# Kernel optimization log

Measured on AMD Instinct MI355X. Metric: run time of the kernel, lower is better.

Reference implementation:

```python
import jax, jax.numpy as jnp
import numpy as np

B, TE, TD, H = 4, 1024, 512, 128


def setup_inputs() -> dict:
    key = jax.random.key(0)
    k1, k2, k3, k4, k5 = jax.random.split(key, 5)
    return {
        "encoder_out": jax.random.normal(k1, (B, TE, H), dtype=jnp.float32),
        "decoder_out": jax.random.normal(k2, (B, TD, H), dtype=jnp.float32),
        "W_a": jax.random.normal(k3, (H, H), dtype=jnp.float32) * 0.05,
        "U_a": jax.random.normal(k4, (H, H), dtype=jnp.float32) * 0.05,
        "V_a": jax.random.normal(k5, (H, 1), dtype=jnp.float32) * 0.05,
    }


def reference(encoder_out, decoder_out, W_a, U_a, V_a):
    # Bahdanau additive attention, vectorized over all decoder steps at once.
    # (The original K.rnn loop has no true recurrence; steps are independent.)
    W_s = jnp.einsum('bth,hk->btk', encoder_out, W_a)   # [B, Te, H]
    U_h = jnp.einsum('bdh,hk->bdk', decoder_out, U_a)   # [B, Td, H]
    # energies: v^T tanh(W s_t + U h_d) -> [B, Td, Te]
    tanh_arg = jnp.tanh(W_s[:, None, :, :] + U_h[:, :, None, :])  # [B, Td, Te, H]
    e = jnp.einsum('bdth,ho->bdt', tanh_arg, V_a)
    e = jax.nn.softmax(e, axis=-1)                      # attention weights [B, Td, Te]
    # context vectors: weighted sum over encoder positions -> [B, Td, H]
    c = jnp.einsum('bdt,bth->bdh', e, encoder_out)
    return (c, e)
```

## Files before the change

kernel.cpp:

```cpp
#include <hip/hip_runtime.h>

#define BB    4
#define TE    1024
#define TD    512
#define HH    128
#define DTILE 4
#define TTILE 64
#define ESTR  (TE + 8)
#define LOG2E 1.4426950408889634f

typedef float f32x2 __attribute__((ext_vector_type(2)));

__device__ __forceinline__ f32x2 pk_fma(f32x2 a, f32x2 b, f32x2 c) {
    return __builtin_elementwise_fma(a, b, c);
}

__device__ __forceinline__ float tanh_eval(float x) {
    float e = __builtin_amdgcn_exp2f(2.0f * LOG2E * x);
    return 1.0f - 2.0f * __builtin_amdgcn_rcpf(e + 1.0f);
}

__global__ __launch_bounds__(256) void proj_gemm(
    const float* __restrict__ enc, const float* __restrict__ dec,
    const float* __restrict__ Wa,  const float* __restrict__ Ua,
    float* __restrict__ out)
{
    __shared__ float Xs[64 * 33];
    __shared__ float Ws[32 * 64];

    const int tid = threadIdx.x;
    const int rt = blockIdx.x >> 1, ch = blockIdx.x & 1;
    const int r0 = rt * 64, c0 = ch * 64;

    const float* X; const float* W; int rX0;
    if (r0 < BB * TE) { X = enc; W = Wa; rX0 = r0; }
    else              { X = dec; W = Ua; rX0 = r0 - BB * TE; }

    const int c4 = tid & 15;
    const int rg = tid >> 4;

    float4 a0 = {0,0,0,0}, a1 = a0, a2 = a0, a3 = a0;

    for (int kc = 0; kc < 4; ++kc) {
        #pragma unroll
        for (int i = 0; i < 2; ++i) {
            int idx = tid + i * 256;
            int r  = idx >> 3, k4 = idx & 7;
            *(float4*)&Xs[r * 33 + k4 * 4] =
                *(const float4*)&X[(rX0 + r) * HH + kc * 32 + k4 * 4];
            int kk = idx >> 4, cc = idx & 15;
            *(float4*)&Ws[kk * 64 + cc * 4] =
                *(const float4*)&W[(kc * 32 + kk) * HH + c0 + cc * 4];
        }
        __syncthreads();
        #pragma unroll 8
        for (int k = 0; k < 32; ++k) {
            float4 wv = *(const float4*)&Ws[k * 64 + c4 * 4];
            float x0 = Xs[(rg * 4 + 0) * 33 + k];
            float x1 = Xs[(rg * 4 + 1) * 33 + k];
            float x2 = Xs[(rg * 4 + 2) * 33 + k];
            float x3 = Xs[(rg * 4 + 3) * 33 + k];
            a0.x = fmaf(x0, wv.x, a0.x); a0.y = fmaf(x0, wv.y, a0.y);
            a0.z = fmaf(x0, wv.z, a0.z); a0.w = fmaf(x0, wv.w, a0.w);
            a1.x = fmaf(x1, wv.x, a1.x); a1.y = fmaf(x1, wv.y, a1.y);
            a1.z = fmaf(x1, wv.z, a1.z); a1.w = fmaf(x1, wv.w, a1.w);
            a2.x = fmaf(x2, wv.x, a2.x); a2.y = fmaf(x2, wv.y, a2.y);
            a2.z = fmaf(x2, wv.z, a2.z); a2.w = fmaf(x2, wv.w, a2.w);
            a3.x = fmaf(x3, wv.x, a3.x); a3.y = fmaf(x3, wv.y, a3.y);
            a3.z = fmaf(x3, wv.z, a3.z); a3.w = fmaf(x3, wv.w, a3.w);
        }
        __syncthreads();
    }

    float4 accs[4] = {a0, a1, a2, a3};
    #pragma unroll
    for (int j = 0; j < 4; ++j) {
        float4 o = accs[j];
        o.x = tanh_eval(o.x); o.y = tanh_eval(o.y);
        o.z = tanh_eval(o.z); o.w = tanh_eval(o.w);
        *(float4*)&out[(r0 + rg * 4 + j) * HH + c0 + c4 * 4] = o;
    }
}

__global__ __launch_bounds__(512, 4) void attn_fused(
    const float* __restrict__ enc,
    const float* __restrict__ ta,
    const float* __restrict__ tb,
    const float* __restrict__ Va,
    float* __restrict__ c_out,
    float* __restrict__ e_out)
{
    __shared__ float e_s[DTILE * ESTR];
    __shared__ float c_red[8 * DTILE * HH];

    const int tid = threadIdx.x;
    const int l   = tid & 63;
    const int w   = tid >> 6;
    const int b   = blockIdx.x >> 7;
    const int d0  = (blockIdx.x & 127) * DTILE;

    {
        const int g  = l >> 3;
        const int hl = l & 7;
        const int dl = g & 3;
        const int rh = g >> 2;

        f32x2 Bl[4], Bh[4], Pl[4], Ph[4], Vl[4], Vh[4];
        #pragma unroll
        for (int j = 0; j < 4; ++j) {
            float4 vv = *(const float4*)&Va[(j * 8 + hl) * 4];
            float4 bb = *(const float4*)&tb[((size_t)b * TD + d0 + dl) * HH + (j * 8 + hl) * 4];
            Vl[j] = (f32x2){vv.x, vv.y};  Vh[j] = (f32x2){vv.z, vv.w};
            Bl[j] = (f32x2){bb.x, bb.y};  Bh[j] = (f32x2){bb.z, bb.w};
            Pl[j] = Vl[j] * Bl[j];        Ph[j] = Vh[j] * Bh[j];
        }

        const float* ta_b = ta + (size_t)b * TE * HH;

        auto rowOf = [&](int i) {
            return ((i >> 2) << 6) + w * 8 + ((i & 3) << 1) + rh;
        };

        float4 A0[4], A1[4];
        auto loadA = [&](int i, float4 (&A)[4]) {
            const float* base = ta_b + (size_t)rowOf(i) * HH;
            #pragma unroll
            for (int j = 0; j < 4; ++j)
                A[j] = *(const float4*)&base[(j * 8 + hl) * 4];
        };

        auto p1c = [&](int i, float4 (&A)[4]) {
            const f32x2 one2 = {1.0f, 1.0f};
            f32x2 n2[8], d2[8];
            #pragma unroll
            for (int j = 0; j < 4; ++j) {
                f32x2 Al = (f32x2){A[j].x, A[j].y};
                f32x2 Ah = (f32x2){A[j].z, A[j].w};
                n2[2 * j]     = pk_fma(Vl[j], Al, Pl[j]);
                n2[2 * j + 1] = pk_fma(Vh[j], Ah, Ph[j]);
                d2[2 * j]     = pk_fma(Al, Bl[j], one2);
                d2[2 * j + 1] = pk_fma(Ah, Bh[j], one2);
            }
            #pragma unroll
            for (int s = 4; s >= 1; s >>= 1) {
                #pragma unroll
                for (int k = 0; k < s; ++k) {
                    n2[k] = pk_fma(n2[2 * k], d2[2 * k + 1], n2[2 * k + 1] * d2[2 * k]);
                    d2[k] = d2[2 * k] * d2[2 * k + 1];
                }
            }
            float num = n2[0].x * d2[0].y + n2[0].y * d2[0].x;
            float den = d2[0].x * d2[0].y;
            float e = num * __builtin_amdgcn_rcpf(den);
            e += __shfl_xor(e, 1);
            e += __shfl_xor(e, 2);
            e += __shfl_xor(e, 4);
            if (hl == 0) e_s[dl * ESTR + rowOf(i)] = e;
        };

        loadA(0, A0);
        #pragma unroll 1
        for (int i = 0; i < 62; i += 2) {
            loadA(i + 1, A1);
            p1c(i, A0);
            loadA(i + 2, A0);
            p1c(i + 1, A1);
        }
        loadA(63, A1);
        p1c(62, A0);
        p1c(63, A1);
    }
    __syncthreads();

    {
        const int d2 = w & 3, hf = w >> 2;
        float ev[16];
        float m = -3.0e38f;
        #pragma unroll
        for (int i = 0; i < 16; ++i) {
            ev[i] = e_s[d2 * ESTR + i * 64 + l];
            m = fmaxf(m, ev[i]);
        }
        #pragma unroll
        for (int off = 32; off; off >>= 1) m = fmaxf(m, __shfl_xor(m, off));
        float s = 0.f;
        #pragma unroll
        for (int i = 0; i < 16; ++i) {
            ev[i] = __builtin_amdgcn_exp2f((ev[i] - m) * LOG2E);
            s += ev[i];
        }
        #pragma unroll
        for (int off = 32; off; off >>= 1) s += __shfl_xor(s, off);
        float inv = __builtin_amdgcn_rcpf(s);

        __syncthreads();
        float* eo = e_out + ((size_t)b * TD + d0 + d2) * TE;
        #pragma unroll
        for (int i = 0; i < 8; ++i) {
            int ii = hf * 8 + i;
            float p = ev[ii] * inv;
            e_s[d2 * ESTR + ii * 64 + l] = p;
            eo[ii * 64 + l] = p;
        }
        __syncthreads();
    }

    const int h4 = l & 31, tsub = l >> 5;
    f32x2 accL[DTILE], accH[DTILE];
    #pragma unroll
    for (int d = 0; d < DTILE; ++d) {
        accL[d] = (f32x2){0.f, 0.f};
        accH[d] = (f32x2){0.f, 0.f};
    }

    {
        const float* enc_w = enc + ((size_t)b * TE + w * 8) * HH;
        float4 X0[4], X1[4];

        auto loadX = [&](int tt, float4 (&X)[4]) {
            const float* base = enc_w + (size_t)tt * TTILE * HH;
            #pragma unroll
            for (int k = 0; k < 4; ++k)
                X[k] = *(const float4*)&base[(tsub * 4 + k) * HH + h4 * 4];
        };

        auto p3c = [&](int tt, float4 (&X)[4]) {
            float4 ep[DTILE];
            #pragma unroll
            for (int d = 0; d < DTILE; ++d)
                ep[d] = *(const float4*)&e_s[d * ESTR + tt * TTILE + w * 8 + tsub * 4];
            #pragma unroll
            for (int k = 0; k < 4; ++k) {
                f32x2 xL = (f32x2){X[k].x, X[k].y};
                f32x2 xH = (f32x2){X[k].z, X[k].w};
                #pragma unroll
                for (int d = 0; d < DTILE; ++d) {
                    float p = k == 0 ? ep[d].x : k == 1 ? ep[d].y
                            : k == 2 ? ep[d].z : ep[d].w;
                    f32x2 pv = (f32x2){p, p};
                    accL[d] = pk_fma(pv, xL, accL[d]);
                    accH[d] = pk_fma(pv, xH, accH[d]);
                }
            }
        };

        loadX(0, X0);
        #pragma unroll 1
        for (int tt = 0; tt < 14; tt += 2) {
            loadX(tt + 1, X1);
            p3c(tt, X0);
            loadX(tt + 2, X0);
            p3c(tt + 1, X1);
        }
        loadX(15, X1);
        p3c(14, X0);
        p3c(15, X1);
    }

    float4 acc4[DTILE];
    #pragma unroll
    for (int d = 0; d < DTILE; ++d)
        acc4[d] = make_float4(accL[d].x, accL[d].y, accH[d].x, accH[d].y);
    #pragma unroll
    for (int d = 0; d < DTILE; ++d) {
        acc4[d].x += __shfl_xor(acc4[d].x, 32);
        acc4[d].y += __shfl_xor(acc4[d].y, 32);
        acc4[d].z += __shfl_xor(acc4[d].z, 32);
        acc4[d].w += __shfl_xor(acc4[d].w, 32);
    }
    if (tsub == 0) {
        #pragma unroll
        for (int d = 0; d < DTILE; ++d)
            *(float4*)&c_red[(w * DTILE + d) * HH + h4 * 4] = acc4[d];
    }
    __syncthreads();

    if (w < DTILE && l < 32) {
        float4 o = make_float4(0.f, 0.f, 0.f, 0.f);
        #pragma unroll
        for (int ww = 0; ww < 8; ++ww) {
            float4 p = *(const float4*)&c_red[(ww * DTILE + w) * HH + l * 4];
            o.x += p.x; o.y += p.y; o.z += p.z; o.w += p.w;
        }
        *(float4*)&c_out[((size_t)b * TD + d0 + w) * HH + l * 4] = o;
    }
}

extern "C" void kernel_launch(void* const* d_in, const int* in_sizes, int n_in,
                              void* d_out, int out_size, void* d_ws, size_t ws_size,
                              hipStream_t stream) {
    (void)in_sizes; (void)n_in; (void)out_size; (void)ws_size;

    const float* enc = (const float*)d_in[0];
    const float* dec = (const float*)d_in[1];
    const float* Wa  = (const float*)d_in[2];
    const float* Ua  = (const float*)d_in[3];
    const float* Va  = (const float*)d_in[4];

    float* c_out = (float*)d_out;
    float* e_out = (float*)d_out + BB * TD * HH;

    float* proj = (float*)d_ws;
    float* ta_p = proj;
    float* tb_p = proj + BB * TE * HH;

    proj_gemm<<<192, 256, 0, stream>>>(enc, dec, Wa, Ua, proj);
    attn_fused<<<(BB * TD) / DTILE, 512, 0, stream>>>(enc, ta_p, tb_p, Va, c_out, e_out);
}
```

Measured before the change: 121.7 us.

## Restructure projection GEMM to 16-row tiles reading weights from global

The projection GEMM now stages only a 16-row slice of X in shared memory and has each thread compute one row by four columns, reading W directly from global memory (relying on cache) with packed FMAs. It launches 384 blocks of 512 threads instead of 192 blocks of 256, removing the K-chunk loop and its repeated barriers. This is meant to raise parallelism and cut synchronization in the small prologue GEMM. In exchange, reuse of W per thread drops and global load traffic for W rises.

After: 131.0 us. +7.7%, slower.

```diff
diff --git a/kernel.cpp b/kernel.cpp
--- a/kernel.cpp
+++ b/kernel.cpp
@@ -20,66 +20,61 @@
     return 1.0f - 2.0f * __builtin_amdgcn_rcpf(e + 1.0f);
 }
 
-__global__ __launch_bounds__(256) void proj_gemm(
+__global__ __launch_bounds__(512) void proj_gemm(
     const float* __restrict__ enc, const float* __restrict__ dec,
     const float* __restrict__ Wa,  const float* __restrict__ Ua,
     float* __restrict__ out)
 {
-    __shared__ float Xs[64 * 33];
-    __shared__ float Ws[32 * 64];
+    __shared__ float Xs[16 * HH];
 
     const int tid = threadIdx.x;
-    const int rt = blockIdx.x >> 1, ch = blockIdx.x & 1;
-    const int r0 = rt * 64, c0 = ch * 64;
+    const int r0  = blockIdx.x * 16;
 
     const float* X; const float* W; int rX0;
     if (r0 < BB * TE) { X = enc; W = Wa; rX0 = r0; }
     else              { X = dec; W = Ua; rX0 = r0 - BB * TE; }
 
-    const int c4 = tid & 15;
-    const int rg = tid >> 4;
-
-    float4 a0 = {0,0,0,0}, a1 = a0, a2 = a0, a3 = a0;
-
-    for (int kc = 0; kc < 4; ++kc) {
-        #pragma unroll
-        for (int i = 0; i < 2; ++i) {
-            int idx = tid + i * 256;
-            int r  = idx >> 3, k4 = idx & 7;
-            *(float4*)&Xs[r * 33 + k4 * 4] =
-                *(const float4*)&X[(rX0 + r) * HH + kc * 32 + k4 * 4];
-            int kk = idx >> 4, cc = idx & 15;
-            *(float4*)&Ws[kk * 64 + cc * 4] =
-                *(const float4*)&W[(kc * 32 + kk) * HH + c0 + cc * 4];
-        }
-        __syncthreads();
-        #pragma unroll 8
-        for (int k = 0; k < 32; ++k) {
-            float4 wv = *(const float4*)&Ws[k * 64 + c4 * 4];
-            float x0 = Xs[(rg * 4 + 0) * 33 + k];
-            float x1 = Xs[(rg * 4 + 1) * 33 + k];
-            float x2 = Xs[(rg * 4 + 2) * 33 + k];
-            float x3 = Xs[(rg * 4 + 3) * 33 + k];
-            a0.x = fmaf(x0, wv.x, a0.x); a0.y = fmaf(x0, wv.y, a0.y);
-            a0.z = fmaf(x0, wv.z, a0.z); a0.w = fmaf(x0, wv.w, a0.w);
-            a1.x = fmaf(x1, wv.x, a1.x); a1.y = fmaf(x1, wv.y, a1.y);
-            a1.z = fmaf(x1, wv.z, a1.z); a1.w = fmaf(x1, wv.w, a1.w);
-            a2.x = fmaf(x2, wv.x, a2.x); a2.y = fmaf(x2, wv.y, a2.y);
-            a2.z = fmaf(x2, wv.z, a2.z); a2.w = fmaf(x2, wv.w, a2.w);
-            a3.x = fmaf(x3, wv.x, a3.x); a3.y = fmaf(x3, wv.y, a3.y);
-            a3.z = fmaf(x3, wv.z, a3.z); a3.w = fmaf(x3, wv.w, a3.w);
-        }
-        __syncthreads();
-    }
-
-    float4 accs[4] = {a0, a1, a2, a3};
-    #pragma unroll
-    for (int j = 0; j < 4; ++j) {
-        float4 o = accs[j];
-        o.x = tanh_eval(o.x); o.y = tanh_eval(o.y);
-        o.z = tanh_eval(o.z); o.w = tanh_eval(o.w);
-        *(float4*)&out[(r0 + rg * 4 + j) * HH + c0 + c4 * 4] = o;
-    }
+    {
+        const int r = tid >> 5, c = tid & 31;
+        *(float4*)&Xs[r * HH + c * 4] =
+            *(const float4*)&X[(size_t)(rX0 + r) * HH + c * 4];
+    }
+    __syncthreads();
+
+    const int rr = tid >> 5;
+    const int c4 = tid & 31;
+
+    f32x2 aL0 = {0.f, 0.f}, aH0 = {0.f, 0.f};
+    f32x2 aL1 = {0.f, 0.f}, aH1 = {0.f, 0.f};
+
+    const float* Wc   = W + c4 * 4;
+    const float* xrow = &Xs[rr * HH];
+
+    #pragma unroll 4
+    for (int k = 0; k < HH; k += 4) {
+        float4 w0 = *(const float4*)&Wc[(k + 0) * HH];
+        float4 w1 = *(const float4*)&Wc[(k + 1) * HH];
+        float4 w2 = *(const float4*)&Wc[(k + 2) * HH];
+        float4 w3 = *(const float4*)&Wc[(k + 3) * HH];
+        float4 xv = *(const float4*)&xrow[k];
+
+        aL0 = pk_fma((f32x2){xv.x, xv.x}, (f32x2){w0.x, w0.y}, aL0);
+        aH0 = pk_fma((f32x2){xv.x, xv.x}, (f32x2){w0.z, w0.w}, aH0);
+        aL1 = pk_fma((f32x2){xv.y, xv.y}, (f32x2){w1.x, w1.y}, aL1);
+        aH1 = pk_fma((f32x2){xv.y, xv.y}, (f32x2){w1.z, w1.w}, aH1);
+        aL0 = pk_fma((f32x2){xv.z, xv.z}, (f32x2){w2.x, w2.y}, aL0);
+        aH0 = pk_fma((f32x2){xv.z, xv.z}, (f32x2){w2.z, w2.w}, aH0);
+        aL1 = pk_fma((f32x2){xv.w, xv.w}, (f32x2){w3.x, w3.y}, aL1);
+        aH1 = pk_fma((f32x2){xv.w, xv.w}, (f32x2){w3.z, w3.w}, aH1);
+    }
+
+    f32x2 aL = aL0 + aL1;
+    f32x2 aH = aH0 + aH1;
+
+    float4 o;
+    o.x = tanh_eval(aL.x); o.y = tanh_eval(aL.y);
+    o.z = tanh_eval(aH.x); o.w = tanh_eval(aH.y);
+    *(float4*)&out[(size_t)(r0 + rr) * HH + c4 * 4] = o;
 }
 
 __global__ __launch_bounds__(512, 4) void attn_fused(
@@ -304,6 +299,6 @@
     float* ta_p = proj;
     float* tb_p = proj + BB * TE * HH;
 
-    proj_gemm<<<192, 256, 0, stream>>>(enc, dec, Wa, Ua, proj);
+    proj_gemm<<<384, 512, 0, stream>>>(enc, dec, Wa, Ua, proj);
     attn_fused<<<(BB * TD) / DTILE, 512, 0, stream>>>(enc, ta_p, tb_p, Va, c_out, e_out);
 }
```
